# Optimization experiments

Hardware: AMD Instinct MI355X
Metric: run time of the kernel (lower is better)

The kernel has to match this reference:

```python
import jax, jax.numpy as jnp
import numpy as np
from jax import lax

K_GROUPS = 4
CH = 256
CG = CH // K_GROUPS  # 64
KK = 9  # 3x3 kernel taps


def setup_inputs() -> dict:
    key = jax.random.key(0)
    ks = jax.random.split(key, 4)
    x = jax.random.normal(ks[0], (16, CH, 64, 64), dtype=jnp.float32)
    # offset-predicting conv: Cg -> 18 (2 offsets per 3x3 tap); small init so offsets are modest
    off_w = jax.random.normal(ks[1], (K_GROUPS, 18, CG, 3, 3), dtype=jnp.float32) * 0.01
    off_b = jnp.zeros((K_GROUPS, 18), dtype=jnp.float32)
    # deformable conv weights: Cg -> Cg, 3x3
    def_w = jax.random.normal(ks[2], (K_GROUPS, CG, CG, 3, 3), dtype=jnp.float32) * (1.0 / np.sqrt(CG * KK))
    def_b = jnp.zeros((K_GROUPS, CG), dtype=jnp.float32)
    return {"x": x, "off_w": off_w, "off_b": off_b, "def_w": def_w, "def_b": def_b}


def _bilinear_sample(img, py, px):
    # img: [B,Cg,H,W]; py,px: [B,KK,H,W] float sample coords -> [B,Cg,KK,H,W]
    B, C, H, W = img.shape
    K = py.shape[1]
    imgf = img.reshape(B, C, H * W)
    y0 = jnp.floor(py)
    x0 = jnp.floor(px)
    wy = py - y0
    wx = px - x0

    def gather(yi, xi, wgt):
        valid = (yi >= 0) & (yi < H) & (xi >= 0) & (xi < W)  # zero padding outside
        yc = jnp.clip(yi, 0, H - 1).astype(jnp.int32)
        xc = jnp.clip(xi, 0, W - 1).astype(jnp.int32)
        idx = (yc * W + xc).reshape(B, 1, K * H * W)
        v = jnp.take_along_axis(imgf, idx, axis=2).reshape(B, C, K, H, W)
        w = (wgt * valid.astype(img.dtype)).reshape(B, 1, K, H, W)
        return v * w

    return (gather(y0, x0, (1 - wy) * (1 - wx))
            + gather(y0, x0 + 1, (1 - wy) * wx)
            + gather(y0 + 1, x0, wy * (1 - wx))
            + gather(y0 + 1, x0 + 1, wy * wx))


def _group_forward(xg, ow, ob, dw, db):
    # xg: [B,Cg,H,W]
    B, C, H, W = xg.shape
    offset = lax.conv_general_dilated(xg, ow, (1, 1), ((1, 1), (1, 1)),
                                      dimension_numbers=("NCHW", "OIHW", "NCHW"))
    offset = offset + ob[None, :, None, None]            # [B,18,H,W]
    off = offset.reshape(B, KK, 2, H, W)                  # per-tap (dy,dx)
    ky, kx = jnp.meshgrid(jnp.arange(-1, 2), jnp.arange(-1, 2), indexing="ij")
    ky = ky.reshape(KK).astype(xg.dtype)
    kx = kx.reshape(KK).astype(xg.dtype)
    hh = jnp.arange(H, dtype=xg.dtype)
    ww = jnp.arange(W, dtype=xg.dtype)
    py = off[:, :, 0] + ky[None, :, None, None] + hh[None, None, :, None]  # [B,KK,H,W]
    px = off[:, :, 1] + kx[None, :, None, None] + ww[None, None, None, :]
    sampled = _bilinear_sample(xg, py, px)                # [B,Cg,KK,H,W]
    out = jnp.einsum("oik,bikhw->bohw", dw.reshape(dw.shape[0], dw.shape[1], KK), sampled)
    return out + db[None, :, None, None]


def reference(x, off_w, off_b, def_w, def_b):
    xs = jnp.split(x, K_GROUPS, axis=1)  # mirrors torch.split over channel groups
    outs = [_group_forward(xs[g], off_w[g], off_b[g], def_w[g], def_b[g])
            for g in range(K_GROUPS)]
    return jnp.concatenate(outs, axis=1)
```

## Files before the change

kernel.cpp:

```cpp
#include <hip/hip_runtime.h>
#include <hip/hip_bf16.h>

#define B_  16
#define G_  4
#define CG  64
#define H_  64
#define W_  64
#define KK  9
#define HW  (H_ * W_)
#define IP  72
#define PD  68
#define XSLICE (PD * PD * CG)

typedef short  short8  __attribute__((ext_vector_type(8)));
typedef float  f32x4   __attribute__((ext_vector_type(4)));
typedef float  f32x16  __attribute__((ext_vector_type(16)));

__device__ __forceinline__ short f2bf(float v) {
    __hip_bfloat16 hb = __float2bfloat16(v);
    short s;
    __builtin_memcpy(&s, &hb, 2);
    return s;
}

__device__ __forceinline__ float2 up2(unsigned int u) {
    union { unsigned int i; float f; } lo, hi;
    lo.i = u << 16;
    hi.i = u & 0xffff0000u;
    return make_float2(lo.f, hi.f);
}

__device__ __forceinline__ unsigned int interp2(unsigned int c00, unsigned int c01,
                                                unsigned int c10, unsigned int c11,
                                                float2 w00, float2 w01,
                                                float2 w10, float2 w11) {
    float2 r = up2(c00) * w00 + up2(c01) * w01 + up2(c10) * w10 + up2(c11) * w11;
    __hip_bfloat162 h = __float22bfloat162_rn(r);
    unsigned int o;
    __builtin_memcpy(&o, &h, 4);
    return o;
}

__global__ void prep_all(const float* __restrict__ x,
                         const float* __restrict__ off_w,
                         const float* __restrict__ def_w,
                         short* __restrict__ xTpad,
                         short* __restrict__ dwA32,
                         short* __restrict__ owA)
{
    const int blk = blockIdx.x;
    const int t   = threadIdx.x;
    __shared__ float sRow[CG][65];

    if (blk < 64 * PD) {
        const int yp = blk % PD;
        const int bg = blk / PD;
        short* dst = xTpad + (size_t)bg * XSLICE + (size_t)yp * PD * CG;

        if (yp < 2 || yp >= 66) {
            const int4 z = {0, 0, 0, 0};
            for (int c = t; c < (PD * CG * 2) / 16; c += 256)
                ((int4*)dst)[c] = z;
            return;
        }

        const int yy = yp - 2;
        const float* src = x + (size_t)bg * CG * HW + (size_t)yy * W_;
        {
            const int i  = t >> 2;
            const int x0 = (t & 3) * 16;
            const float* sp = src + (size_t)i * HW + x0;
#pragma unroll
            for (int c = 0; c < 4; c++) {
                const float4 v = ((const float4*)sp)[c];
                sRow[i][x0 + c * 4 + 0] = v.x;
                sRow[i][x0 + c * 4 + 1] = v.y;
                sRow[i][x0 + c * 4 + 2] = v.z;
                sRow[i][x0 + c * 4 + 3] = v.w;
            }
        }
        __syncthreads();

        for (int task = t; task < PD * 8; task += 256) {
            const int ich = task & 7;
            const int xp  = task >> 3;
            const int xx  = xp - 2;
            short8 v = {0, 0, 0, 0, 0, 0, 0, 0};
            if ((unsigned)xx < (unsigned)W_) {
#pragma unroll
                for (int e = 0; e < 8; e++) v[e] = f2bf(sRow[ich * 8 + e][xx]);
            }
            *(short8*)(dst + xp * CG + ich * 8) = v;
        }
        return;
    }

    const int tid = (blk - 64 * PD) * 256 + t;
    const int ndw = G_ * KK * 4096;
    const int now = G_ * 18 * 2 * 4 * 16 * 8;
    if (tid < ndw) {
        const int e    = tid & 7;
        const int o    = (tid >> 3) & 31;
        const int q2   = (tid >> 8) & 1;
        const int step = (tid >> 9) & 3;
        const int mt   = (tid >> 11) & 1;
        const int gk   = tid >> 12;
        const int k    = gk % KK;
        const int g    = gk / KK;
        const int oo   = mt * 32 + o;
        const int i    = step * 16 + q2 * 8 + e;
        dwA32[tid] = f2bf(def_w[((g * CG + oo) * CG + i) * KK + k]);
    } else if (tid < ndw + now) {
        const int t2 = tid - ndw;
        const int e  = t2 & 7;
        const int jj = (t2 >> 3) & 15;
        const int q  = (t2 >> 7) & 3;
        const int tm = (t2 >> 9) & 1;
        const int gs = t2 >> 10;
        const int s  = gs % 18;
        const int g  = gs / 18;
        const int j  = tm * 16 + jj;
        const int rc = s >> 1;
        const int i  = (s & 1) * 32 + q * 8 + e;
        owA[t2] = (j < 18) ? f2bf(off_w[((g * 18 + j) * CG + i) * KK + rc]) : (short)0;
    }
}

__global__ __launch_bounds__(256, 7)
void deform_main(const short* __restrict__ xTpad,
                 const float* __restrict__ off_b,
                 const float* __restrict__ def_b,
                 const short* __restrict__ dwA32,
                 const short* __restrict__ owA,
                 float* __restrict__ out)
{
    const int raw = blockIdx.x;
    const int r8  = raw & 7;
    const int h   = (raw >> 3) & 63;
    const int q8  = raw >> 9;
    const int bg  = q8 * 8 + r8;
    const int b   = bg >> 2;
    const int g   = bg & 3;

    __shared__ float2 pcs[KK][64];
    __shared__ short  sT[2][64 * IP];

    const int t    = threadIdx.x;
    const int lane = t & 63;
    const int p    = t >> 6;
    const int nn   = lane & 15;
    const int q    = lane >> 4;

    const short* xb = xTpad + (size_t)bg * XSLICE;

    {
        const short* owAg = owA + g * 18 * 1024;
        f32x4 oa0 = {0.f, 0.f, 0.f, 0.f};
        f32x4 oa1 = {0.f, 0.f, 0.f, 0.f};
#pragma unroll
        for (int rc = 0; rc < 9; rc++) {
            const int rr = rc / 3;
            const int cc = rc % 3;
            const short* cp = xb + ((h + rr + 1) * PD + (p * 16 + nn + cc + 1)) * CG + q * 8;
            const short8 b0 = *(const short8*)cp;
            const short8 b1 = *(const short8*)(cp + 32);
            const int s0 = rc * 2, s1 = rc * 2 + 1;
            const short8 a00 = *(const short8*)(owAg + ((s0 * 2 + 0) * 4 + q) * 128 + nn * 8);
            const short8 a01 = *(const short8*)(owAg + ((s0 * 2 + 1) * 4 + q) * 128 + nn * 8);
            const short8 a10 = *(const short8*)(owAg + ((s1 * 2 + 0) * 4 + q) * 128 + nn * 8);
            const short8 a11 = *(const short8*)(owAg + ((s1 * 2 + 1) * 4 + q) * 128 + nn * 8);
            oa0 = __builtin_amdgcn_mfma_f32_16x16x32_bf16(a00, b0, oa0, 0, 0, 0);
            oa1 = __builtin_amdgcn_mfma_f32_16x16x32_bf16(a01, b0, oa1, 0, 0, 0);
            oa0 = __builtin_amdgcn_mfma_f32_16x16x32_bf16(a10, b1, oa0, 0, 0, 0);
            oa1 = __builtin_amdgcn_mfma_f32_16x16x32_bf16(a11, b1, oa1, 0, 0, 0);
        }
        const int n = p * 16 + nn;
#pragma unroll
        for (int reg = 0; reg < 4; reg++) {
            const int j  = q * 4 + reg;
            const int kk = j >> 1;
            const float v = oa0[reg] + off_b[g * 18 + j];
            if ((j & 1) == 0) pcs[kk][n].x = v + (float)(kk / 3) + (float)(h + 1);
            else              pcs[kk][n].y = v + (float)(kk % 3) + (float)(n + 1);
        }
        if (q == 0) {
            pcs[8][n].x = oa1[0] + off_b[g * 18 + 16] + 2.0f + (float)(h + 1);
            pcs[8][n].y = oa1[1] + off_b[g * 18 + 17] + 2.0f + (float)(n + 1);
        }
    }

    const int mt  = p >> 1;
    const int nt  = p & 1;
    const int n31 = lane & 31;
    const int q2  = lane >> 5;

    f32x16 acc = {0.f};
    const short* dwg = dwA32 + g * KK * 4096;

    const int posL  = lane >> 3;
    const int chidx = lane & 7;

    auto gather_tap = [&](int k, short* __restrict__ sTb) {
#pragma unroll
        for (int it = 0; it < 2; it++) {
            const int pos = p * 16 + it * 8 + posL;
            const float2 pc = pcs[k][pos];
            const float yf = floorf(pc.x);
            const float xf = floorf(pc.y);
            const float wy = pc.x - yf;
            const float wx = pc.y - xf;
            int y0 = (int)yf;
            int x0 = (int)xf;
            y0 = (y0 < 0) ? 0 : ((y0 > 66) ? 66 : y0);
            x0 = (x0 < 0) ? 0 : ((x0 > 66) ? 66 : x0);
            const short* cp = xb + (y0 * PD + x0) * CG + chidx * 8;
            const uint4 c00 = *(const uint4*)cp;
            const uint4 c01 = *(const uint4*)(cp + CG);
            const uint4 c10 = *(const uint4*)(cp + PD * CG);
            const uint4 c11 = *(const uint4*)(cp + PD * CG + CG);
            const float a00 = (1.0f - wy) * (1.0f - wx);
            const float a01 = (1.0f - wy) * wx;
            const float a10 = wy * (1.0f - wx);
            const float a11 = wy * wx;
            const float2 w00 = make_float2(a00, a00);
            const float2 w01 = make_float2(a01, a01);
            const float2 w10 = make_float2(a10, a10);
            const float2 w11 = make_float2(a11, a11);
            uint4 ov;
            ov.x = interp2(c00.x, c01.x, c10.x, c11.x, w00, w01, w10, w11);
            ov.y = interp2(c00.y, c01.y, c10.y, c11.y, w00, w01, w10, w11);
            ov.z = interp2(c00.z, c01.z, c10.z, c11.z, w00, w01, w10, w11);
            ov.w = interp2(c00.w, c01.w, c10.w, c11.w, w00, w01, w10, w11);
            *(uint4*)&sTb[pos * IP + chidx * 8] = ov;
        }
    };

    auto einsum_tap = [&](int k, const short* __restrict__ sTb) {
        const short* dwk = dwg + k * 4096;
#pragma unroll
        for (int step = 0; step < 4; step++) {
            const short8 af = *(const short8*)(dwk + ((mt * 4 + step) * 2 + q2) * 256 + n31 * 8);
            const short8 bf = *(const short8*)&sTb[(nt * 32 + n31) * IP + step * 16 + q2 * 8];
            acc = __builtin_amdgcn_mfma_f32_32x32x16_bf16(af, bf, acc, 0, 0, 0);
        }
    };

    gather_tap(0, &sT[0][0]);
    __syncthreads();
    for (int k = 0; k < KK; k++) {
        if (k < KK - 1) gather_tap(k + 1, &sT[(k + 1) & 1][0]);
        einsum_tap(k, &sT[k & 1][0]);
        __syncthreads();
    }

    float* outb = out + (size_t)(b * 256 + g * 64) * HW + h * W_;
    const int n = nt * 32 + n31;
#pragma unroll
    for (int reg = 0; reg < 16; reg++) {
        const int o = mt * 32 + (reg & 3) + 8 * (reg >> 2) + 4 * q2;
        outb[(size_t)o * HW + n] = acc[reg] + def_b[g * 64 + o];
    }
}

__global__ __launch_bounds__(256, 4)
void deform_fallback(const float* __restrict__ x,
                     const float* __restrict__ off_w,
                     const float* __restrict__ off_b,
                     const float* __restrict__ def_w,
                     const float* __restrict__ def_b,
                     float* __restrict__ out)
{
    const int raw = blockIdx.x;
    const int r8  = raw & 7;
    const int h   = (raw >> 3) & 63;
    const int q8  = raw >> 9;
    const int bg  = q8 * 8 + r8;
    const int b   = bg >> 2;
    const int g   = bg & 3;

    __shared__ float pys[KK][W_];
    __shared__ float pxs[KK][W_];
    __shared__ float buf[8192];
    float* red   = buf;
    float* s_lds = buf;
    float* dwTl  = buf + 4096;

    const int t = threadIdx.x;
    const int w = t & 63;
    const int p = t >> 6;

    const float* xg = x + (size_t)(b * 256 + g * 64) * HW;

    float acc[18];
#pragma unroll
    for (int j = 0; j < 18; j++) acc[j] = 0.0f;
    {
        const int i0 = p * 16;
        for (int ii = 0; ii < 16; ii++) {
            const int i = i0 + ii;
            const float* xi = xg + i * HW;
#pragma unroll
            for (int r = 0; r < 3; r++) {
                const int y = h + r - 1;
                if ((unsigned)y >= (unsigned)H_) continue;
#pragma unroll
                for (int c = 0; c < 3; c++) {
                    const int xc = w + c - 1;
                    const float xv = ((unsigned)xc < (unsigned)W_) ? xi[y * W_ + xc] : 0.0f;
#pragma unroll
                    for (int j = 0; j < 18; j++) {
                        const float wv = off_w[((g * 18 + j) * CG + i) * 9 + r * 3 + c];
                        acc[j] = fmaf(wv, xv, acc[j]);
                    }
                }
            }
        }
    }
#pragma unroll
    for (int j = 0; j < 18; j++) red[(p * 18 + j) * 64 + w] = acc[j];
    __syncthreads();
    for (int idx = t; idx < 18 * 64; idx += 256) {
        const int j  = idx >> 6;
        const int ww = idx & 63;
        float v = red[(0 * 18 + j) * 64 + ww] + red[(1 * 18 + j) * 64 + ww]
                + red[(2 * 18 + j) * 64 + ww] + red[(3 * 18 + j) * 64 + ww];
        v += off_b[g * 18 + j];
        const int k = j >> 1;
        if ((j & 1) == 0) pys[k][ww] = v + (float)(k / 3 - 1) + (float)h;
        else              pxs[k][ww] = v + (float)(k % 3 - 1) + (float)ww;
    }
    __syncthreads();

    float facc[16];
#pragma unroll
    for (int qd = 0; qd < 16; qd++) facc[qd] = 0.0f;
    const int w4 = (t & 15) << 2;
    const int o4 = (t >> 4) << 2;

    for (int k = 0; k < KK; k++) {
#pragma unroll
        for (int n = 0; n < 16; n++) {
            const int v = t + 256 * n;
            const int i = v >> 6;
            const int o = v & 63;
            dwTl[v] = def_w[((g * CG + o) * CG + i) * KK + k];
        }
        const float py  = pys[k][w];
        const float px  = pxs[k][w];
        const float y0f = floorf(py);
        const float x0f = floorf(px);
        const float wy  = py - y0f;
        const float wx  = px - x0f;
        const int   y0  = (int)y0f;
        const int   x0  = (int)x0f;
        const float w00 = (1.0f - wy) * (1.0f - wx);
        const float w01 = (1.0f - wy) * wx;
        const float w10 = wy * (1.0f - wx);
        const float w11 = wy * wx;
        const bool vy0 = (unsigned)y0       < (unsigned)H_;
        const bool vy1 = (unsigned)(y0 + 1) < (unsigned)H_;
        const bool vx0 = (unsigned)x0       < (unsigned)W_;
        const bool vx1 = (unsigned)(x0 + 1) < (unsigned)W_;
        const int a00 = y0 * W_ + x0;
#pragma unroll
        for (int n = 0; n < 16; n++) {
            const int i = (n << 2) + p;
            const float* xi = xg + i * HW;
            const float v00 = (vy0 && vx0) ? xi[a00]          : 0.0f;
            const float v01 = (vy0 && vx1) ? xi[a00 + 1]      : 0.0f;
            const float v10 = (vy1 && vx0) ? xi[a00 + W_]     : 0.0f;
            const float v11 = (vy1 && vx1) ? xi[a00 + W_ + 1] : 0.0f;
            s_lds[i * 64 + w] = w00 * v00 + w01 * v01 + w10 * v10 + w11 * v11;
        }
        __syncthreads();
#pragma unroll 4
        for (int i = 0; i < CG; i++) {
            const float4 sv = *(const float4*)&s_lds[i * 64 + w4];
            const float4 dv = *(const float4*)&dwTl[i * 64 + o4];
            facc[0]  = fmaf(dv.x, sv.x, facc[0]);
            facc[1]  = fmaf(dv.x, sv.y, facc[1]);
            facc[2]  = fmaf(dv.x, sv.z, facc[2]);
            facc[3]  = fmaf(dv.x, sv.w, facc[3]);
            facc[4]  = fmaf(dv.y, sv.x, facc[4]);
            facc[5]  = fmaf(dv.y, sv.y, facc[5]);
            facc[6]  = fmaf(dv.y, sv.z, facc[6]);
            facc[7]  = fmaf(dv.y, sv.w, facc[7]);
            facc[8]  = fmaf(dv.z, sv.x, facc[8]);
            facc[9]  = fmaf(dv.z, sv.y, facc[9]);
            facc[10] = fmaf(dv.z, sv.z, facc[10]);
            facc[11] = fmaf(dv.z, sv.w, facc[11]);
            facc[12] = fmaf(dv.w, sv.x, facc[12]);
            facc[13] = fmaf(dv.w, sv.y, facc[13]);
            facc[14] = fmaf(dv.w, sv.z, facc[14]);
            facc[15] = fmaf(dv.w, sv.w, facc[15]);
        }
        __syncthreads();
    }

    float* outp = out + (size_t)(b * 256 + g * 64) * HW + h * W_;
#pragma unroll
    for (int oo = 0; oo < 4; oo++) {
        const int o = o4 + oo;
        const float bias = def_b[g * 64 + o];
        float4 r;
        r.x = facc[oo * 4 + 0] + bias;
        r.y = facc[oo * 4 + 1] + bias;
        r.z = facc[oo * 4 + 2] + bias;
        r.w = facc[oo * 4 + 3] + bias;
        *(float4*)&outp[o * HW + w4] = r;
    }
}

extern "C" void kernel_launch(void* const* d_in, const int* in_sizes, int n_in,
                              void* d_out, int out_size, void* d_ws, size_t ws_size,
                              hipStream_t stream)
{
    (void)in_sizes; (void)n_in; (void)out_size;
    const float* x     = (const float*)d_in[0];
    const float* off_w = (const float*)d_in[1];
    const float* off_b = (const float*)d_in[2];
    const float* def_w = (const float*)d_in[3];
    const float* def_b = (const float*)d_in[4];
    float* out = (float*)d_out;

    const size_t xT_bytes  = (size_t)B_ * G_ * XSLICE * 2;
    const size_t dw_bytes  = (size_t)G_ * KK * 4096 * 2;
    const size_t ow_bytes  = (size_t)G_ * 18 * 1024 * 2;
    const size_t need = xT_bytes + dw_bytes + ow_bytes;

    const int nblk   = B_ * G_ * H_;
    const int nprepw = (G_ * KK * 4096 + G_ * 18 * 1024 + 255) / 256;
    const int nprep  = 64 * PD + nprepw;

    if (ws_size >= need) {
        short* xTpad = (short*)d_ws;
        short* dwA32 = (short*)((char*)d_ws + xT_bytes);
        short* owA   = (short*)((char*)d_ws + xT_bytes + dw_bytes);
        prep_all<<<nprep, 256, 0, stream>>>(x, off_w, def_w, xTpad, dwA32, owA);
        deform_main<<<nblk, 256, 0, stream>>>(xTpad, off_b, def_b, dwA32, owA, out);
    } else {
        deform_fallback<<<nblk, 256, 0, stream>>>(x, off_w, off_b, def_w, def_b, out);
    }
}
```

Baseline: 224.3 us.

## Feed bilinear samples directly into MFMA registers, dropping LDS staging

Measured after the change: 317.2 us. 41.4% more time.

```diff
diff --git a/kernel.cpp b/kernel.cpp
--- a/kernel.cpp
+++ b/kernel.cpp
@@ -8,13 +8,11 @@
 #define W_  64
 #define KK  9
 #define HW  (H_ * W_)
-#define IP  72
 #define PD  68
 #define XSLICE (PD * PD * CG)
 
 typedef short  short8  __attribute__((ext_vector_type(8)));
 typedef float  f32x4   __attribute__((ext_vector_type(4)));
-typedef float  f32x16  __attribute__((ext_vector_type(16)));
 
 __device__ __forceinline__ short f2bf(float v) {
     __hip_bfloat16 hb = __float2bfloat16(v);
@@ -41,11 +39,24 @@
     return o;
 }
 
+__device__ __forceinline__ short8 interp8(uint4 a, uint4 b, uint4 c, uint4 d,
+                                          float2 w00, float2 w01,
+                                          float2 w10, float2 w11) {
+    uint4 r;
+    r.x = interp2(a.x, b.x, c.x, d.x, w00, w01, w10, w11);
+    r.y = interp2(a.y, b.y, c.y, d.y, w00, w01, w10, w11);
+    r.z = interp2(a.z, b.z, c.z, d.z, w00, w01, w10, w11);
+    r.w = interp2(a.w, b.w, c.w, d.w, w00, w01, w10, w11);
+    short8 s;
+    __builtin_memcpy(&s, &r, 16);
+    return s;
+}
+
 __global__ void prep_all(const float* __restrict__ x,
                          const float* __restrict__ off_w,
                          const float* __restrict__ def_w,
                          short* __restrict__ xTpad,
-                         short* __restrict__ dwA32,
+                         short* __restrict__ dwE,
                          short* __restrict__ owA)
 {
     const int blk = blockIdx.x;
@@ -99,17 +110,17 @@
     const int ndw = G_ * KK * 4096;
     const int now = G_ * 18 * 2 * 4 * 16 * 8;
     if (tid < ndw) {
-        const int e    = tid & 7;
-        const int o    = (tid >> 3) & 31;
-        const int q2   = (tid >> 8) & 1;
-        const int step = (tid >> 9) & 3;
-        const int mt   = (tid >> 11) & 1;
-        const int gk   = tid >> 12;
-        const int k    = gk % KK;
-        const int g    = gk / KK;
-        const int oo   = mt * 32 + o;
-        const int i    = step * 16 + q2 * 8 + e;
-        dwA32[tid] = f2bf(def_w[((g * CG + oo) * CG + i) * KK + k]);
+        const int e  = tid & 7;
+        const int nn = (tid >> 3) & 15;
+        const int q  = (tid >> 7) & 3;
+        const int kh = (tid >> 9) & 1;
+        const int ot = (tid >> 10) & 3;
+        const int gk = tid >> 12;
+        const int k  = gk % KK;
+        const int g  = gk / KK;
+        const int o  = ot * 16 + nn;
+        const int i  = kh * 32 + q * 8 + e;
+        dwE[tid] = f2bf(def_w[((g * CG + o) * CG + i) * KK + k]);
     } else if (tid < ndw + now) {
         const int t2 = tid - ndw;
         const int e  = t2 & 7;
@@ -126,11 +137,11 @@
     }
 }
 
-__global__ __launch_bounds__(256, 7)
+__global__ __launch_bounds__(256, 4)
 void deform_main(const short* __restrict__ xTpad,
                  const float* __restrict__ off_b,
                  const float* __restrict__ def_b,
-                 const short* __restrict__ dwA32,
+                 const short* __restrict__ dwE,
                  const short* __restrict__ owA,
                  float* __restrict__ out)
 {
@@ -143,7 +154,6 @@
     const int g   = bg & 3;
 
     __shared__ float2 pcs[KK][64];
-    __shared__ short  sT[2][64 * IP];
 
     const int t    = threadIdx.x;
     const int lane = t & 63;
@@ -189,76 +199,65 @@
         }
     }
 
-    const int mt  = p >> 1;
-    const int nt  = p & 1;
-    const int n31 = lane & 31;
-    const int q2  = lane >> 5;
-
-    f32x16 acc = {0.f};
-    const short* dwg = dwA32 + g * KK * 4096;
-
-    const int posL  = lane >> 3;
-    const int chidx = lane & 7;
-
-    auto gather_tap = [&](int k, short* __restrict__ sTb) {
-#pragma unroll
-        for (int it = 0; it < 2; it++) {
-            const int pos = p * 16 + it * 8 + posL;
-            const float2 pc = pcs[k][pos];
-            const float yf = floorf(pc.x);
-            const float xf = floorf(pc.y);
-            const float wy = pc.x - yf;
-            const float wx = pc.y - xf;
-            int y0 = (int)yf;
-            int x0 = (int)xf;
-            y0 = (y0 < 0) ? 0 : ((y0 > 66) ? 66 : y0);
-            x0 = (x0 < 0) ? 0 : ((x0 > 66) ? 66 : x0);
-            const short* cp = xb + (y0 * PD + x0) * CG + chidx * 8;
-            const uint4 c00 = *(const uint4*)cp;
-            const uint4 c01 = *(const uint4*)(cp + CG);
-            const uint4 c10 = *(const uint4*)(cp + PD * CG);
-            const uint4 c11 = *(const uint4*)(cp + PD * CG + CG);
-            const float a00 = (1.0f - wy) * (1.0f - wx);
-            const float a01 = (1.0f - wy) * wx;
-            const float a10 = wy * (1.0f - wx);
-            const float a11 = wy * wx;
-            const float2 w00 = make_float2(a00, a00);
-            const float2 w01 = make_float2(a01, a01);
-            const float2 w10 = make_float2(a10, a10);
-            const float2 w11 = make_float2(a11, a11);
-            uint4 ov;
-            ov.x = interp2(c00.x, c01.x, c10.x, c11.x, w00, w01, w10, w11);
-            ov.y = interp2(c00.y, c01.y, c10.y, c11.y, w00, w01, w10, w11);
-            ov.z = interp2(c00.z, c01.z, c10.z, c11.z, w00, w01, w10, w11);
-            ov.w = interp2(c00.w, c01.w, c10.w, c11.w, w00, w01, w10, w11);
-            *(uint4*)&sTb[pos * IP + chidx * 8] = ov;
-        }
-    };
-
-    auto einsum_tap = [&](int k, const short* __restrict__ sTb) {
-        const short* dwk = dwg + k * 4096;
-#pragma unroll
-        for (int step = 0; step < 4; step++) {
-            const short8 af = *(const short8*)(dwk + ((mt * 4 + step) * 2 + q2) * 256 + n31 * 8);
-            const short8 bf = *(const short8*)&sTb[(nt * 32 + n31) * IP + step * 16 + q2 * 8];
-            acc = __builtin_amdgcn_mfma_f32_32x32x16_bf16(af, bf, acc, 0, 0, 0);
-        }
-    };
-
-    gather_tap(0, &sT[0][0]);
-    __syncthreads();
+    const int pos = p * 16 + nn;
+
+    f32x4 acc[4];
+#pragma unroll
+    for (int ot = 0; ot < 4; ot++) acc[ot] = (f32x4){0.f, 0.f, 0.f, 0.f};
+
+    const short* dwl = dwE + g * KK * 4096 + q * 128 + nn * 8;
+
     for (int k = 0; k < KK; k++) {
-        if (k < KK - 1) gather_tap(k + 1, &sT[(k + 1) & 1][0]);
-        einsum_tap(k, &sT[k & 1][0]);
-        __syncthreads();
+        const float2 pc = pcs[k][pos];
+        const float yf = floorf(pc.x);
+        const float xf = floorf(pc.y);
+        const float wy = pc.x - yf;
+        const float wx = pc.y - xf;
+        int y0 = (int)yf;
+        int x0 = (int)xf;
+        y0 = (y0 < 0) ? 0 : ((y0 > 66) ? 66 : y0);
+        x0 = (x0 < 0) ? 0 : ((x0 > 66) ? 66 : x0);
+        const short* cp = xb + (y0 * PD + x0) * CG + q * 8;
+
+        const uint4 a00 = *(const uint4*)(cp);
+        const uint4 a01 = *(const uint4*)(cp + CG);
+        const uint4 a10 = *(const uint4*)(cp + PD * CG);
+        const uint4 a11 = *(const uint4*)(cp + PD * CG + CG);
+        const uint4 b00 = *(const uint4*)(cp + 32);
+        const uint4 b01 = *(const uint4*)(cp + CG + 32);
+        const uint4 b10 = *(const uint4*)(cp + PD * CG + 32);
+        const uint4 b11 = *(const uint4*)(cp + PD * CG + CG + 32);
+
+        const float s00 = (1.0f - wy) * (1.0f - wx);
+        const float s01 = (1.0f - wy) * wx;
+        const float s10 = wy * (1.0f - wx);
+        const float s11 = wy * wx;
+        const float2 w00 = make_float2(s00, s00);
+        const float2 w01 = make_float2(s01, s01);
+        const float2 w10 = make_float2(s10, s10);
+        const float2 w11 = make_float2(s11, s11);
+
+        const short8 bf0 = interp8(a00, a01, a10, a11, w00, w01, w10, w11);
+        const short8 bf1 = interp8(b00, b01, b10, b11, w00, w01, w10, w11);
+
+        const short* dwk = dwl + k * 4096;
+#pragma unroll
+        for (int ot = 0; ot < 4; ot++) {
+            const short8 af0 = *(const short8*)(dwk + ot * 1024);
+            const short8 af1 = *(const short8*)(dwk + ot * 1024 + 512);
+            acc[ot] = __builtin_amdgcn_mfma_f32_16x16x32_bf16(af0, bf0, acc[ot], 0, 0, 0);
+            acc[ot] = __builtin_amdgcn_mfma_f32_16x16x32_bf16(af1, bf1, acc[ot], 0, 0, 0);
+        }
     }
 
     float* outb = out + (size_t)(b * 256 + g * 64) * HW + h * W_;
-    const int n = nt * 32 + n31;
-#pragma unroll
-    for (int reg = 0; reg < 16; reg++) {
-        const int o = mt * 32 + (reg & 3) + 8 * (reg >> 2) + 4 * q2;
-        outb[(size_t)o * HW + n] = acc[reg] + def_b[g * 64 + o];
+#pragma unroll
+    for (int ot = 0; ot < 4; ot++) {
+#pragma unroll
+        for (int reg = 0; reg < 4; reg++) {
+            const int o = ot * 16 + q * 4 + reg;
+            outb[(size_t)o * HW + pos] = acc[ot][reg] + def_b[g * 64 + o];
+        }
     }
 }
 
@@ -434,10 +433,10 @@
 
     if (ws_size >= need) {
         short* xTpad = (short*)d_ws;
-        short* dwA32 = (short*)((char*)d_ws + xT_bytes);
+        short* dwE   = (short*)((char*)d_ws + xT_bytes);
         short* owA   = (short*)((char*)d_ws + xT_bytes + dw_bytes);
-        prep_all<<<nprep, 256, 0, stream>>>(x, off_w, def_w, xTpad, dwA32, owA);
-        deform_main<<<nblk, 256, 0, stream>>>(xTpad, off_b, def_b, dwA32, owA, out);
+        prep_all<<<nprep, 256, 0, stream>>>(x, off_w, def_w, xTpad, dwE, owA);
+        deform_main<<<nblk, 256, 0, stream>>>(xTpad, off_b, def_b, dwE, owA, out);
     } else {
         deform_fallback<<<nblk, 256, 0, stream>>>(x, off_w, off_b, def_w, def_b, out);
     }
```
